# Optimization experiments

Measured on AMD Instinct MI355X. Metric: run time of the kernel, lower is better.

The kernel has to match this reference:

```python
import jax, jax.numpy as jnp
import numpy as np


def setup_inputs() -> dict:
    key = jax.random.key(0)
    k1, k2 = jax.random.split(key)
    B, D, H, W = 32, 64, 32, 32
    K = 1024
    z_e = jax.random.normal(k1, (B, D, H, W), dtype=jnp.float32)
    # original init: uniform(-1/K, 1/K); use same scale
    emb = jax.random.uniform(k2, (K, D), dtype=jnp.float32, minval=-1.0 / K, maxval=1.0 / K)
    return {"z_e": z_e, "emb": emb}


COMMITMENT_COST = 0.25


def reference(z_e, emb):
    # z_e: [B, D, H, W], emb: [K, D]
    B, D, H, W = z_e.shape
    K = emb.shape[0]
    z = jnp.transpose(z_e, (0, 2, 3, 1))           # [B, H, W, D]
    flat = z.reshape(-1, D)                        # [N, D]
    N = flat.shape[0]

    dist = (
        jnp.sum(flat * flat, axis=1, keepdims=True)
        + jnp.sum(emb * emb, axis=1)
        - 2.0 * flat @ emb.T
    )
    idx = jnp.argmin(dist, axis=1)                 # [N]
    encodings = jax.nn.one_hot(idx, K, dtype=flat.dtype)  # [N, K]
    z_q = (encodings @ emb).reshape(z.shape)       # [B, H, W, D]

    e_latent_loss = jnp.mean((jax.lax.stop_gradient(z_q) - z) ** 2)
    q_latent_loss = jnp.mean((z_q - jax.lax.stop_gradient(z)) ** 2)
    loss = q_latent_loss + COMMITMENT_COST * e_latent_loss

    # straight-through estimator
    z_st = z + jax.lax.stop_gradient(z_q - z)

    avg_probs = jnp.sum(encodings, axis=0) / jnp.float32(N)
    perplexity = jnp.exp(-jnp.sum(avg_probs * jnp.log(avg_probs + 1e-10)))

    return (jnp.transpose(z_st, (0, 3, 1, 2)), loss, perplexity, encodings)
```

## Files before the change

kernel.cpp:

```cpp
#include <hip/hip_runtime.h>
#include <stdint.h>
#include <math.h>

constexpr int Kk  = 1024;

constexpr int OUT0_N   = 32 * 64 * 1024;
constexpr int OUT_LOSS = OUT0_N;
constexpr int OUT_PERP = OUT0_N + 1;
constexpr int OUT_ENC  = OUT0_N + 2;

constexpr size_t WS_CNT = 0;
constexpr size_t WS_LP  = 4096;
constexpr size_t WS_MBN = 12288;
constexpr size_t WS_KEY = 16384;

typedef short bf16x8 __attribute__((ext_vector_type(8)));
typedef float f32x16 __attribute__((ext_vector_type(16)));

__device__ __forceinline__ float norm64v(const float4* __restrict__ p) {
#pragma clang fp contract(off)
    float tt[64];
#pragma unroll
    for (int q = 0; q < 16; ++q) {
        float4 v = p[q];
        tt[4 * q + 0] = v.x * v.x;
        tt[4 * q + 1] = v.y * v.y;
        tt[4 * q + 2] = v.z * v.z;
        tt[4 * q + 3] = v.w * v.w;
    }
    float r[8];
#pragma unroll
    for (int j = 0; j < 8; ++j) r[j] = tt[j];
#pragma unroll
    for (int i = 8; i < 64; i += 8)
#pragma unroll
        for (int j = 0; j < 8; ++j) r[j] += tt[i + j];
    return ((r[0] + r[1]) + (r[2] + r[3])) + ((r[4] + r[5]) + (r[6] + r[7]));
}

__device__ __forceinline__ uint32_t fsort(float f) {
    uint32_t b = __float_as_uint(f);
    return (b & 0x80000000u) ? ~b : (b | 0x80000000u);
}

__device__ __forceinline__ unsigned short f2bf(float f) {
    uint32_t u = __float_as_uint(f);
    uint32_t r = (u + 0x7fffu + ((u >> 16) & 1u)) >> 16;
    return (unsigned short)r;
}

__device__ __forceinline__ unsigned long long
exact_key(float A, const float* __restrict__ xr, const float* __restrict__ emb,
          uint32_t code) {
    const float* er = emb + (size_t)code * 64;
    float C = 0.f;
#pragma unroll
    for (int d = 0; d < 64; ++d) C = __builtin_fmaf(xr[d], er[d], C);
    float Bv = norm64v((const float4*)er);
    float s = A + Bv;
    float dist = __builtin_fmaf(-2.f, C, s);
    return ((unsigned long long)fsort(dist) << 32) | code;
}

__global__ __launch_bounds__(256, 4)
void dist_mfma(const float* __restrict__ z_e, const float* __restrict__ emb,
               unsigned long long* __restrict__ lockey,
               uint32_t* __restrict__ counts,
               float* __restrict__ maxbn,
               float* __restrict__ out) {
    __shared__ unsigned short xbf[128 * 64];
    __shared__ unsigned short ebf[128 * 64];
    __shared__ float Bn_s[128];
    __shared__ float xsqp[2][128];
    __shared__ float mbn_s;
    const int t = threadIdx.x, lane = t & 63, wv = t >> 6, g = lane >> 5;
    const int rg = blockIdx.x >> 3, cg = blockIdx.x & 7;
    const int n0 = rg * 128, b = n0 >> 10, hw0 = n0 & 1023;
    const float* zb = z_e + (size_t)b * 65536 + hw0;

    {
        int hwi = t & 127, d4g = t >> 7;
        float xq = 0.f;
#pragma unroll
        for (int it = 0; it < 8; ++it) {
            int dbase = (d4g + it * 2) * 4;
            float v0 = zb[(size_t)(dbase + 0) * 1024 + hwi];
            float v1 = zb[(size_t)(dbase + 1) * 1024 + hwi];
            float v2 = zb[(size_t)(dbase + 2) * 1024 + hwi];
            float v3 = zb[(size_t)(dbase + 3) * 1024 + hwi];
            xq = __builtin_fmaf(v0, v0, xq);
            xq = __builtin_fmaf(v1, v1, xq);
            xq = __builtin_fmaf(v2, v2, xq);
            xq = __builtin_fmaf(v3, v3, xq);
            ushort4 bv;
            bv.x = f2bf(v0); bv.y = f2bf(v1); bv.z = f2bf(v2); bv.w = f2bf(v3);
            *(ushort4*)((char*)xbf + hwi * 128 + ((dbase * 2) ^ ((hwi & 7) << 4))) = bv;
        }
        xsqp[d4g][hwi] = xq;
    }
    {
        const float4* ep = (const float4*)(emb + (size_t)cg * 8192);
#pragma unroll
        for (int it = 0; it < 8; ++it) {
            int j = t + it * 256;
            float4 v = ep[j];
            int code = j >> 4, q = j & 15;
            ushort4 bv;
            bv.x = f2bf(v.x); bv.y = f2bf(v.y); bv.z = f2bf(v.z); bv.w = f2bf(v.w);
            *(ushort4*)((char*)ebf + code * 128 + ((q * 8) ^ ((code & 7) << 4))) = bv;
        }
    }
    if (t < 128) Bn_s[t] = norm64v((const float4*)(emb + (size_t)(cg * 128 + t) * 64));
    if (blockIdx.x == 0) ((uint4*)counts)[t] = make_uint4(0u, 0u, 0u, 0u);
    __syncthreads();
    if (wv == 0) {
        float m = fmaxf(Bn_s[lane], Bn_s[lane + 64]);
#pragma unroll
        for (int s = 1; s < 64; s <<= 1) m = fmaxf(m, __shfl_xor(m, s, 64));
        if (lane == 0) { mbn_s = m; if (rg == 0) maxbn[cg] = m; }
    }
    __syncthreads();

    const int rowl = wv * 32 + (lane & 31);
    const float xsq = xsqp[0][rowl] + xsqp[1][rowl];
    const float margin = 0.017f * sqrtf(xsq * mbn_s) + 1.0e-4f;

    const int swz = (lane & 7) << 4;
    bf16x8 bfr[4];
    const char* xb = (const char*)xbf + rowl * 128;
#pragma unroll
    for (int s = 0; s < 4; ++s)
        bfr[s] = *(const bf16x8*)(xb + ((s * 32 + g * 16) ^ swz));
    const char* ebase = (const char*)ebf + (lane & 31) * 128;

    float4* encz = (float4*)(out + OUT_ENC) + (size_t)blockIdx.x * 4096;
    const float4 zero4 = make_float4(0.f, 0.f, 0.f, 0.f);

    float runmin = 3.4e38f;
#pragma unroll 1
    for (int tm = 0; tm < 4; ++tm) {
        encz[(size_t)(tm * 2 + 0) * 256 + t] = zero4;
        encz[(size_t)(tm * 2 + 1) * 256 + t] = zero4;
        const char* p = ebase + tm * 4096;
        f32x16 acc = {};
#pragma unroll
        for (int s = 0; s < 4; ++s)
            acc = __builtin_amdgcn_mfma_f32_32x32x16_bf16(
                *(const bf16x8*)(p + ((s * 32 + g * 16) ^ swz)), bfr[s], acc, 0, 0, 0);
#pragma unroll
        for (int r = 0; r < 16; ++r) {
            int cl = tm * 32 + (r & 3) + 8 * (r >> 2) + 4 * g;
            runmin = fminf(runmin, __builtin_fmaf(-2.f, acc[r], Bn_s[cl]));
        }
    }
    runmin = fminf(runmin, __shfl_xor(runmin, 32, 64));
    const float thr = runmin + margin;

    uint32_t cnt = 0, c0 = 0, c1 = 0, c2 = 0;
#pragma unroll 1
    for (int tm = 0; tm < 4; ++tm) {
        encz[(size_t)(8 + tm * 2 + 0) * 256 + t] = zero4;
        encz[(size_t)(8 + tm * 2 + 1) * 256 + t] = zero4;
        const char* p = ebase + tm * 4096;
        f32x16 acc = {};
#pragma unroll
        for (int s = 0; s < 4; ++s)
            acc = __builtin_amdgcn_mfma_f32_32x32x16_bf16(
                *(const bf16x8*)(p + ((s * 32 + g * 16) ^ swz)), bfr[s], acc, 0, 0, 0);
#pragma unroll
        for (int r = 0; r < 16; ++r) {
            int cl = tm * 32 + (r & 3) + 8 * (r >> 2) + 4 * g;
            float sv = __builtin_fmaf(-2.f, acc[r], Bn_s[cl]);
            if (sv <= thr) {
                uint32_t gc = (uint32_t)(cg * 128 + cl);
                if (cnt == 0u) c0 = gc; else if (cnt == 1u) c1 = gc; else if (cnt == 2u) c2 = gc;
                ++cnt;
            }
        }
    }
    uint32_t pc = __shfl_xor(cnt, 32, 64);
    uint32_t p0 = __shfl_xor(c0, 32, 64);
    uint32_t p1 = __shfl_xor(c1, 32, 64);
    uint32_t p2 = __shfl_xor(c2, 32, 64);
    if (lane < 32) {
        uint32_t tot = cnt + pc;
        uint32_t lo;
        if (tot > 3u || tot == 0u) {
            lo = 3u << 30;
        } else {
            uint32_t a0 = c0, a1 = c1, a2 = c2;
            if (cnt == 0u)      { a0 = p0; a1 = p1; a2 = p2; }
            else if (cnt == 1u) { a1 = p0; a2 = p1; }
            else if (cnt == 2u) { a2 = p0; }
            if (tot < 2u) a1 = 0u;
            if (tot < 3u) a2 = 0u;
            lo = ((tot - 1u) << 30) | (a0 & 1023u) | ((a1 & 1023u) << 10) | ((a2 & 1023u) << 20);
        }
        unsigned long long key = ((unsigned long long)__float_as_uint(runmin) << 32) | lo;
        lockey[(size_t)(n0 + rowl) * 8 + cg] = key;
    }
}

__global__ __launch_bounds__(256)
void finish_kernel(const float* __restrict__ z_e,
                   const float* __restrict__ emb,
                   const unsigned long long* __restrict__ lockey,
                   const float* __restrict__ maxbn,
                   uint32_t* __restrict__ counts,
                   double* __restrict__ lp,
                   float* __restrict__ out) {
    __shared__ float zs[32 * 68];
    __shared__ uint32_t scode[32];
    __shared__ double lred[4];
    const int t = threadIdx.x;
    const int n0 = blockIdx.x * 32;
    const int b = n0 >> 10, hw0 = n0 & 1023;
    const int hwi = t & 31, dg = t >> 5;
    const size_t base = (size_t)b * 65536 + (size_t)(dg * 8) * 1024 + hw0 + hwi;

    float zreg[8];
#pragma unroll
    for (int k = 0; k < 8; ++k) zreg[k] = z_e[base + (size_t)k * 1024];
#pragma unroll
    for (int m = 0; m < 2; ++m)
        *(float4*)&zs[hwi * 68 + dg * 8 + 4 * m] =
            make_float4(zreg[4 * m], zreg[4 * m + 1], zreg[4 * m + 2], zreg[4 * m + 3]);
    __syncthreads();

    if (t < 32) {
        const unsigned long long* k8 = lockey + (size_t)(n0 + t) * 8;
        unsigned long long kw0 = k8[0], kw1 = k8[1], kw2 = k8[2], kw3 = k8[3];
        unsigned long long kw4 = k8[4], kw5 = k8[5], kw6 = k8[6], kw7 = k8[7];
        unsigned long long kws[8] = {kw0, kw1, kw2, kw3, kw4, kw5, kw6, kw7};
        float gmin = 3.4e38f;
#pragma unroll
        for (int i = 0; i < 8; ++i)
            gmin = fminf(gmin, __uint_as_float((uint32_t)(kws[i] >> 32)));
        const float* xr = &zs[t * 68];
        float A = norm64v((const float4*)xr);
        float mb = maxbn[0];
#pragma unroll
        for (int i = 1; i < 8; ++i) mb = fmaxf(mb, maxbn[i]);
        const float thr = gmin + 0.017f * sqrtf(A * mb) + 1.0e-4f;

        int nc = 0; uint32_t first = 0; bool ovf = false;
#pragma unroll
        for (int i = 0; i < 8; ++i) {
            float f = __uint_as_float((uint32_t)(kws[i] >> 32));
            if (f > thr) continue;
            uint32_t lo = (uint32_t)kws[i], cc = lo >> 30;
            if (cc == 3u) ovf = true;
            else { nc += (int)cc + 1; first = lo & 1023u; }
        }
        uint32_t code;
        if (!ovf && nc == 1) {
            code = first;
        } else {
            unsigned long long best = ~0ULL;
#pragma unroll
            for (int i = 0; i < 8; ++i) {
                float f = __uint_as_float((uint32_t)(kws[i] >> 32));
                if (f > thr) continue;
                uint32_t lo = (uint32_t)kws[i], cc = lo >> 30;
                if (cc == 3u) {
#pragma unroll 1
                    for (int c = 0; c < 128; ++c) {
                        unsigned long long key = exact_key(A, xr, emb, (uint32_t)(i * 128 + c));
                        best = (key < best) ? key : best;
                    }
                } else {
#pragma unroll 1
                    for (uint32_t q = 0; q <= cc; ++q) {
                        unsigned long long key = exact_key(A, xr, emb, (lo >> (10u * q)) & 1023u);
                        best = (key < best) ? key : best;
                    }
                }
            }
            code = (uint32_t)best;
        }
        scode[t] = code;
        atomicAdd(&counts[code], 1u);
        out[(size_t)OUT_ENC + (size_t)(n0 + t) * 1024 + code] = 1.0f;
    }
    __syncthreads();

    {
        const uint32_t code = scode[hwi];
        const float4* er4 = (const float4*)(emb + (size_t)code * 64) + dg * 2;
        double ls = 0.0;
#pragma unroll
        for (int k4 = 0; k4 < 2; ++k4) {
            float4 e4 = er4[k4];
            float f0 = e4.x, f1 = e4.y, f2 = e4.z, f3 = e4.w;
            size_t off = base + (size_t)(k4 * 4) * 1024;
            {
                float z = zreg[k4 * 4 + 0]; float tt = f0 - z;
                out[off] = z + tt;              ls += (double)tt * (double)tt;
            }
            {
                float z = zreg[k4 * 4 + 1]; float tt = f1 - z;
                out[off + 1024] = z + tt;       ls += (double)tt * (double)tt;
            }
            {
                float z = zreg[k4 * 4 + 2]; float tt = f2 - z;
                out[off + 2048] = z + tt;       ls += (double)tt * (double)tt;
            }
            {
                float z = zreg[k4 * 4 + 3]; float tt = f3 - z;
                out[off + 3072] = z + tt;       ls += (double)tt * (double)tt;
            }
        }
#pragma unroll
        for (int m = 32; m >= 1; m >>= 1) ls += __shfl_down(ls, m, 64);
        if ((t & 63) == 0) lred[t >> 6] = ls;
    }
    __syncthreads();
    if (t == 0) lp[blockIdx.x] = lred[0] + lred[1] + lred[2] + lred[3];
}

__global__ void scalar_kernel(const uint32_t* __restrict__ counts,
                              const double* __restrict__ lp,
                              float* __restrict__ out) {
    __shared__ double redl[4], redh[4];
    const int t = threadIdx.x;
    double ls = 0.0;
    for (int i = t; i < 1024; i += 256) ls += lp[i];
    double h = 0.0;
    for (int i = t; i < Kk; i += 256) {
        double p = (double)counts[i] * (1.0 / 32768.0);
        h += p * log(p + 1e-10);
    }
#pragma unroll
    for (int m = 32; m >= 1; m >>= 1) { ls += __shfl_down(ls, m, 64); h += __shfl_down(h, m, 64); }
    if ((t & 63) == 0) { redl[t >> 6] = ls; redh[t >> 6] = h; }
    __syncthreads();
    if (t == 0) {
        double L = redl[0] + redl[1] + redl[2] + redl[3];
        double H = redh[0] + redh[1] + redh[2] + redh[3];
        out[OUT_PERP] = (float)exp(-H);
        float m32 = (float)(L * (1.0 / 2097152.0));
        out[OUT_LOSS] = m32 + 0.25f * m32;
    }
}

extern "C" void kernel_launch(void* const* d_in, const int* in_sizes, int n_in,
                              void* d_out, int out_size, void* d_ws, size_t ws_size,
                              hipStream_t stream) {
    const float* z_e = (const float*)d_in[0];
    const float* emb = (const float*)d_in[1];
    float* out = (float*)d_out;
    char* ws = (char*)d_ws;

    uint32_t* counts = (uint32_t*)(ws + WS_CNT);
    double*   lp     = (double*)(ws + WS_LP);
    float*    mbn    = (float*)(ws + WS_MBN);
    unsigned long long* lockey = (unsigned long long*)(ws + WS_KEY);

    dist_mfma<<<2048, 256, 0, stream>>>(z_e, emb, lockey, counts, mbn, out);
    finish_kernel<<<1024, 256, 0, stream>>>(z_e, emb, lockey, mbn, counts, lp, out);
    scalar_kernel<<<1, 256, 0, stream>>>(counts, lp, out);
}
```

Baseline: 244.5 us.

## Parallelize exact-distance candidate refinement across the whole block in finish kernel

Candidate rescoring in the finish kernel used to run serially inside the 32 threads of one wavefront, with overflow rows scanning 128 codes each. Candidate (row, code) pairs are now collected into a shared list and scored by all 256 threads. Overflow rows, and rows with more than six candidates, scan all 1024 codes cooperatively using a wave shuffle reduction. This cuts the serial tail from rows with ambiguous argmins but adds shared-memory bookkeeping and extra barriers.

```diff
diff --git a/kernel.cpp b/kernel.cpp
--- a/kernel.cpp
+++ b/kernel.cpp
@@ -210,14 +210,30 @@
                    double* __restrict__ lp,
                    float* __restrict__ out) {
     __shared__ float zs[32 * 68];
+    __shared__ float arow[32];
     __shared__ uint32_t scode[32];
+    __shared__ uint8_t ncarr[32];
+    __shared__ unsigned long long pkey[32][6];
+    __shared__ uint32_t pairbuf[192];
+    __shared__ uint32_t ovfbuf[32];
+    __shared__ uint32_t npairs, novf;
+    __shared__ float mbg_s;
+    __shared__ unsigned long long rbuf[4];
     __shared__ double lred[4];
-    const int t = threadIdx.x;
+    const int t = threadIdx.x, lane = t & 63, wv = t >> 6;
     const int n0 = blockIdx.x * 32;
     const int b = n0 >> 10, hw0 = n0 & 1023;
     const int hwi = t & 31, dg = t >> 5;
     const size_t base = (size_t)b * 65536 + (size_t)(dg * 8) * 1024 + hw0 + hwi;
 
+    if (t == 0) {
+        npairs = 0u; novf = 0u;
+        float mb = maxbn[0];
+#pragma unroll
+        for (int i = 1; i < 8; ++i) mb = fmaxf(mb, maxbn[i]);
+        mbg_s = mb;
+    }
+
     float zreg[8];
 #pragma unroll
     for (int k = 0; k < 8; ++k) zreg[k] = z_e[base + (size_t)k * 1024];
@@ -229,60 +245,100 @@
 
     if (t < 32) {
         const unsigned long long* k8 = lockey + (size_t)(n0 + t) * 8;
-        unsigned long long kw0 = k8[0], kw1 = k8[1], kw2 = k8[2], kw3 = k8[3];
-        unsigned long long kw4 = k8[4], kw5 = k8[5], kw6 = k8[6], kw7 = k8[7];
-        unsigned long long kws[8] = {kw0, kw1, kw2, kw3, kw4, kw5, kw6, kw7};
+        unsigned long long kws[8];
+#pragma unroll
+        for (int i = 0; i < 8; ++i) kws[i] = k8[i];
         float gmin = 3.4e38f;
 #pragma unroll
         for (int i = 0; i < 8; ++i)
             gmin = fminf(gmin, __uint_as_float((uint32_t)(kws[i] >> 32)));
-        const float* xr = &zs[t * 68];
-        float A = norm64v((const float4*)xr);
-        float mb = maxbn[0];
-#pragma unroll
-        for (int i = 1; i < 8; ++i) mb = fmaxf(mb, maxbn[i]);
-        const float thr = gmin + 0.017f * sqrtf(A * mb) + 1.0e-4f;
-
-        int nc = 0; uint32_t first = 0; bool ovf = false;
+        float A = norm64v((const float4*)&zs[t * 68]);
+        arow[t] = A;
+        const float thr = gmin + 0.017f * sqrtf(A * mbg_s) + 1.0e-4f;
+
+        int nc = 0; uint32_t cand[6]; bool ovf = false;
 #pragma unroll
         for (int i = 0; i < 8; ++i) {
             float f = __uint_as_float((uint32_t)(kws[i] >> 32));
             if (f > thr) continue;
             uint32_t lo = (uint32_t)kws[i], cc = lo >> 30;
-            if (cc == 3u) ovf = true;
-            else { nc += (int)cc + 1; first = lo & 1023u; }
-        }
-        uint32_t code;
-        if (!ovf && nc == 1) {
-            code = first;
+            if (cc == 3u) { ovf = true; }
+            else {
+#pragma unroll
+                for (uint32_t q = 0; q < 3u; ++q)
+                    if (q <= cc) {
+                        if (nc < 6) cand[nc] = (lo >> (10u * q)) & 1023u;
+                        ++nc;
+                    }
+            }
+        }
+        if (ovf || nc > 6 || nc == 0) {
+            ncarr[t] = 255u;
+            ovfbuf[atomicAdd(&novf, 1u)] = (uint32_t)t;
+        } else if (nc == 1) {
+            ncarr[t] = 1u;
+            scode[t] = cand[0];
         } else {
-            unsigned long long best = ~0ULL;
-#pragma unroll
-            for (int i = 0; i < 8; ++i) {
-                float f = __uint_as_float((uint32_t)(kws[i] >> 32));
-                if (f > thr) continue;
-                uint32_t lo = (uint32_t)kws[i], cc = lo >> 30;
-                if (cc == 3u) {
+            ncarr[t] = (uint8_t)nc;
+            uint32_t bs = atomicAdd(&npairs, (uint32_t)nc);
+#pragma unroll
+            for (int q = 0; q < 6; ++q)
+                if (q < nc)
+                    pairbuf[bs + q] = ((uint32_t)t << 13) | ((uint32_t)q << 10) | cand[q];
+        }
+    }
+    __syncthreads();
+
+    for (uint32_t p = t; p < npairs; p += 256u) {
+        uint32_t pk = pairbuf[p];
+        int row = (int)(pk >> 13), slot = (int)((pk >> 10) & 7u);
+        pkey[row][slot] = exact_key(arow[row], &zs[row * 68], emb, pk & 1023u);
+    }
+    __syncthreads();
+
+    for (uint32_t o = 0; o < novf; ++o) {
+        int row = (int)ovfbuf[o];
+        const float* xr = &zs[row * 68];
+        float A = arow[row];
+        unsigned long long best = ~0ULL;
 #pragma unroll 1
-                    for (int c = 0; c < 128; ++c) {
-                        unsigned long long key = exact_key(A, xr, emb, (uint32_t)(i * 128 + c));
-                        best = (key < best) ? key : best;
-                    }
-                } else {
-#pragma unroll 1
-                    for (uint32_t q = 0; q <= cc; ++q) {
-                        unsigned long long key = exact_key(A, xr, emb, (lo >> (10u * q)) & 1023u);
-                        best = (key < best) ? key : best;
-                    }
-                }
-            }
-            code = (uint32_t)best;
-        }
-        scode[t] = code;
+        for (int cq = 0; cq < 4; ++cq) {
+            unsigned long long key = exact_key(A, xr, emb, (uint32_t)(t + cq * 256));
+            best = (key < best) ? key : best;
+        }
+#pragma unroll
+        for (int m = 1; m < 64; m <<= 1) {
+            unsigned long long ok = __shfl_xor(best, m, 64);
+            best = (ok < best) ? ok : best;
+        }
+        if (lane == 0) rbuf[wv] = best;
+        __syncthreads();
+        if (t == 0) {
+            unsigned long long bb = rbuf[0];
+#pragma unroll
+            for (int w = 1; w < 4; ++w) bb = (rbuf[w] < bb) ? rbuf[w] : bb;
+            scode[row] = (uint32_t)bb;
+        }
+        __syncthreads();
+    }
+
+    if (t < 32) {
+        uint8_t nc = ncarr[t];
+        if (nc >= 2u && nc != 255u) {
+            unsigned long long bb = pkey[t][0];
+#pragma unroll
+            for (int q = 1; q < 6; ++q)
+                if (q < (int)nc && pkey[t][q] < bb) bb = pkey[t][q];
+            scode[t] = (uint32_t)bb;
+        }
+    }
+    __syncthreads();
+
+    if (t < 32) {
+        uint32_t code = scode[t];
         atomicAdd(&counts[code], 1u);
         out[(size_t)OUT_ENC + (size_t)(n0 + t) * 1024 + code] = 1.0f;
     }
-    __syncthreads();
 
     {
         const uint32_t code = scode[hwi];
```

Result: faster. 199.6 us (-18.4%).
